# Performance work log

Measured on AMD Instinct MI355X. Metric: run time of the kernel, lower is better.

The kernel has to match this reference:

```python
import jax, jax.numpy as jnp
import numpy as np

N2 = 128      # time horizon (days)
M = 16384     # number of regions / batched chains
START = 6     # seeding window (days with externally seeded cases)


def setup_inputs() -> dict:
    key = jax.random.key(0)
    k0, k1, k2, k3, k4 = jax.random.split(key, 5)
    # reproduction numbers R_t in [0, 2)
    rt = jax.random.uniform(k0, (N2, M), dtype=jnp.float32) * 2.0
    deaths_gt = jax.random.uniform(k1, (N2, M), dtype=jnp.float32)
    # serial-interval distribution (positive, sums to 1 so the recurrence stays bounded)
    si_raw = jax.random.uniform(k2, (N2,), dtype=jnp.float32)
    SI = si_raw / jnp.sum(si_raw)
    f_raw = jax.random.uniform(k3, (N2, M), dtype=jnp.float32)
    f = f_raw / jnp.sum(f_raw, axis=0, keepdims=True) * 0.01
    # seeded cases for the first START days
    seed = jax.random.uniform(k4, (START, M), dtype=jnp.float32)
    return {"rt": rt, "deaths_gt": deaths_gt, "SI": SI, "f": f,
            "seed": seed, "start": START}


def _predict_cases(rt, SI, seed, start):
    # prediction[i, m] = rt[i, m] * sum_{j < i} prediction[j, m] * SI[i - j]
    # sequential triangular recurrence over time -> lax.scan with full carry.
    n2, m = rt.shape
    idx = jnp.arange(n2)
    pred0 = jnp.zeros((n2, m), rt.dtype).at[:start].set(seed)

    def step(pred, i):
        d = i - idx                                   # SI lag for each j
        w = jnp.where(d > 0, SI[jnp.clip(d, 0, n2 - 1)], 0.0)  # [N2], zero for j >= i
        conv = w @ pred                               # [M]
        row = jnp.where(i >= start, rt[i] * conv, pred[i])
        return pred.at[i].set(row), None

    pred, _ = jax.lax.scan(step, pred0, jnp.arange(n2))
    return pred


def _predict_deaths(pred, f, start):
    # E_deaths[i, m] = sum_{j <= i-2} pred[j, m] * f[i-j, m]
    # = causal per-region convolution with lags d = i-j >= 2 (so zero f[0], f[1]).
    n2, m = pred.shape
    f_eff = f.at[:2].set(0.0)
    conv = jax.vmap(lambda p, k: jnp.convolve(p, k)[:n2],
                    in_axes=1, out_axes=1)(pred, f_eff)   # [N2, M]
    i = jnp.arange(n2)[:, None]
    # rows before `start` are untouched by the loop (0), row 0 is set to 1e-9
    return jnp.where(i >= start, conv, jnp.where(i == 0, 1e-9, 0.0))


def reference(rt, deaths_gt, SI, f, seed, start):
    cases_pred = _predict_cases(rt, SI, seed, start)
    deaths_pred = _predict_deaths(cases_pred, f, start)
    return jnp.mean((deaths_pred - deaths_gt) ** 2)  # nn.MSELoss
```

## Files before the change

kernel.cpp:

```cpp
#include <hip/hip_runtime.h>

#define N2 128
#define MM 16384
#define START 6
#define CB 32
#define BT 256
#define PROWS 132
#define FROWS 152

__global__ __launch_bounds__(BT, 4) void npi_fused(
    const float* __restrict__ rt, const float* __restrict__ dgt,
    const float* __restrict__ si, const float* __restrict__ f,
    const float* __restrict__ seed, float* __restrict__ out)
{
    __shared__ float predT[PROWS * CB];
    __shared__ float funion[FROWS * CB];
    __shared__ float si_s[N2];
    __shared__ float lred[4];
    float* part = funion;
    float* fTd  = funion;

    const int t = threadIdx.x;
    const int c = t & (CB - 1);
    const int w = t >> 6;
    const int g = t >> 5;
    const int hw = g & 1;
    const int m = blockIdx.x * CB + c;

    float fregs[16];
#pragma unroll
    for (int q = 0; q < 16; ++q)
        fregs[q] = f[((g << 4) + q) * MM + m];

    if (t < N2) si_s[t] = si[t];
    if (g < START) predT[(g << 5) + c] = seed[g * MM + m];
    if (g < 4) predT[((128 + g) << 5) + c] = 0.f;

    float r16v[16];
#pragma unroll
    for (int k = 0; k < 16; ++k)
        r16v[k] = rt[k * MM + m];

    __syncthreads();

    float sr[16];
#pragma unroll
    for (int k = 1; k < 16; ++k) sr[k] = si_s[k];

    {
        float p_[16], v[16];
#pragma unroll
        for (int k = 0; k < 16; ++k) p_[k] = 0.f;
#pragma unroll
        for (int k = 0; k < 16; ++k) {
            float vk;
            if (k < START) vk = predT[(k << 5) + c];
            else vk = r16v[k] * (p_[k] + sr[1] * v[k - 1]);
            v[k] = vk;
#pragma unroll
            for (int k2 = k + 2; k2 < 16; ++k2)
                p_[k2] += sr[k2 - k] * vk;
        }
        if (w == 3 && hw == 0) {
#pragma unroll
            for (int k = START; k < 16; ++k) predT[(k << 5) + c] = v[k];
        }
    }
    __syncthreads();

    for (int b = 1; b < 8; ++b) {
        const int i0 = b << 4;
        const int nst = b << 1;
#pragma unroll
        for (int k = 0; k < 16; ++k)
            r16v[k] = rt[(i0 + k) * MM + m];

        const int jhi = nst * (g + 1);
        const int base = i0 - jhi + 1;
        float c16[16];
#pragma unroll
        for (int e = 0; e < 16; ++e) c16[e] = si_s[base + e];
        float acc[16];
#pragma unroll
        for (int k = 0; k < 16; ++k) acc[k] = 0.f;
#pragma unroll
        for (int u = 0; u < 14; ++u) {
            if (u < nst) {
                float p = predT[((jhi - 1 - u) << 5) + c];
#pragma unroll
                for (int k = 0; k < 16; ++k)
                    acc[k] += p * c16[(u + k) & 15];
                if (u + 1 < nst) c16[u & 15] = si_s[base + 16 + u];
            }
        }
#pragma unroll
        for (int k = 0; k < 16; ++k)
            acc[k] += __shfl_xor(acc[k], 32, 64);
        if (hw == 0) {
#pragma unroll
            for (int k = 0; k < 16; ++k)
                part[(((w << 4) + k) << 5) + c] = acc[k];
        }
        __syncthreads();

        float p_[16], v[16];
#pragma unroll
        for (int k = 0; k < 16; ++k)
            p_[k] = part[(k << 5) + c] + part[((16 + k) << 5) + c]
                  + part[((32 + k) << 5) + c] + part[((48 + k) << 5) + c];
#pragma unroll
        for (int k = 0; k < 16; ++k) {
            float vk = (k == 0) ? (r16v[0] * p_[0])
                                : (r16v[k] * (p_[k] + sr[1] * v[k - 1]));
            v[k] = vk;
#pragma unroll
            for (int k2 = k + 2; k2 < 16; ++k2)
                p_[k2] += sr[k2 - k] * vk;
        }
        {
            float a0, a1;
            if (w == 0)      { a0 = hw ? v[2]  : v[0];  a1 = hw ? v[3]  : v[1];  }
            else if (w == 1) { a0 = hw ? v[6]  : v[4];  a1 = hw ? v[7]  : v[5];  }
            else if (w == 2) { a0 = hw ? v[10] : v[8];  a1 = hw ? v[11] : v[9];  }
            else             { a0 = hw ? v[14] : v[12]; a1 = hw ? v[15] : v[13]; }
            const int r0 = i0 + (w << 2) + (hw << 1);
            predT[(r0 << 5) + c] = a0;
            predT[((r0 + 1) << 5) + c] = a1;
        }
        __syncthreads();
    }

#pragma unroll
    for (int q = 0; q < 16; ++q) {
        int d = (g << 4) + q;
        fTd[((16 + d) << 5) + c] = (d < 2) ? 0.f : fregs[q];
    }
    fTd[((g << 1) << 5) + c] = 0.f;
    fTd[(((g << 1) + 1) << 5) + c] = 0.f;
    fTd[((144 + g) << 5) + c] = 0.f;
    __syncthreads();

    float lsum = 0.f;
    if (hw == 0) {
        float dv = dgt[w * MM + m];
        float e0 = (w == 0) ? (1e-9f - dv) : dv;
        lsum += e0 * e0;
        if (w < 2) {
            float d2 = dgt[(4 + w) * MM + m];
            lsum += d2 * d2;
        }
    }

#pragma unroll
    for (int pass = 0; pass < 2; ++pass) {
        const int n = pass ? (7 - w) : w;
        const int i0 = START + (n << 4);
        const int jhi2 = i0 + 14;
        const int steps = jhi2 >> 1;
        const int jh = hw ? jhi2 : (jhi2 >> 1);
        const int fb = 17 + i0 - jh;

        float dg[16];
#pragma unroll
        for (int k = 0; k < 16; ++k)
            dg[k] = (i0 + k < N2) ? dgt[(i0 + k) * MM + m] : 0.f;

        float cf[16];
#pragma unroll
        for (int e = 0; e < 16; ++e) cf[e] = fTd[((fb + e) << 5) + c];
        float acc[16];
#pragma unroll
        for (int k = 0; k < 16; ++k) acc[k] = 0.f;

        for (int sb = 0; sb < steps; sb += 16) {
#pragma unroll
            for (int u = 0; u < 16; ++u) {
                int s = sb + u;
                if (s < steps) {
                    float p = predT[((jh - 1 - s) << 5) + c];
#pragma unroll
                    for (int k = 0; k < 16; ++k)
                        acc[k] += p * cf[(u + k) & 15];
                    cf[u] = fTd[((fb + 16 + s) << 5) + c];
                }
            }
        }
#pragma unroll
        for (int k = 0; k < 16; ++k)
            acc[k] += __shfl_xor(acc[k], 32, 64);
        if (hw == 0) {
#pragma unroll
            for (int k = 0; k < 16; ++k) {
                if (i0 + k < N2) {
                    float diff = acc[k] - dg[k];
                    lsum += diff * diff;
                }
            }
        }
    }

#pragma unroll
    for (int off = 32; off > 0; off >>= 1)
        lsum += __shfl_down(lsum, off, 64);
    if ((t & 63) == 0) lred[w] = lsum;
    __syncthreads();
    if (t == 0)
        atomicAdd(out, (lred[0] + lred[1] + lred[2] + lred[3]) *
                       (1.0f / ((float)N2 * (float)MM)));
}

extern "C" void kernel_launch(void* const* d_in, const int* in_sizes, int n_in,
                              void* d_out, int out_size, void* d_ws, size_t ws_size,
                              hipStream_t stream) {
    const float* rt   = (const float*)d_in[0];
    const float* dgt  = (const float*)d_in[1];
    const float* si   = (const float*)d_in[2];
    const float* f    = (const float*)d_in[3];
    const float* seed = (const float*)d_in[4];

    hipMemsetAsync(d_out, 0, sizeof(float), stream);
    npi_fused<<<dim3(MM / CB), dim3(BT), 0, stream>>>(
        rt, dgt, si, f, seed, (float*)d_out);
}
```

Before: 107.1 us.

## Halve columns per block and split convolution work four ways per column

Columns per block drop from 32 to 16, so each column is handled by 16 threads instead of 8. The j-range of the case and death convolutions is split four ways within a wavefront and reduced with two xor shuffles. The cross-wave partial sum moves into a separate shared-memory reduction pass with an extra barrier. Each thread now recomputes the 16-step recurrence but writes only one row, and loads of seed, death targets and f are spread across more threads. The intent is to double the number of blocks and cut the serial per-thread work for more parallelism and latency hiding, at the cost of more barriers, more shuffles and redundant recurrence work.

```diff
diff --git a/kernel.cpp b/kernel.cpp
--- a/kernel.cpp
+++ b/kernel.cpp
@@ -3,43 +3,42 @@
 #define N2 128
 #define MM 16384
 #define START 6
-#define CB 32
+#define CB 16
 #define BT 256
-#define PROWS 132
-#define FROWS 152
 
 __global__ __launch_bounds__(BT, 4) void npi_fused(
     const float* __restrict__ rt, const float* __restrict__ dgt,
     const float* __restrict__ si, const float* __restrict__ f,
     const float* __restrict__ seed, float* __restrict__ out)
 {
-    __shared__ float predT[PROWS * CB];
-    __shared__ float funion[FROWS * CB];
+    __shared__ float predT[132 * CB];
+    __shared__ float funion[152 * CB];
     __shared__ float si_s[N2];
     __shared__ float lred[4];
-    float* part = funion;
-    float* fTd  = funion;
 
     const int t = threadIdx.x;
-    const int c = t & (CB - 1);
+    const int c = t & 15;
+    const int s = (t >> 4) & 1;
+    const int h = (t >> 5) & 1;
     const int w = t >> 6;
-    const int g = t >> 5;
-    const int hw = g & 1;
+    const int q = (h << 1) | s;
+    const int g = (h << 3) | (w << 1) | s;
     const int m = blockIdx.x * CB + c;
 
-    float fregs[16];
-#pragma unroll
-    for (int q = 0; q < 16; ++q)
-        fregs[q] = f[((g << 4) + q) * MM + m];
+    float fregs[8];
+#pragma unroll
+    for (int r = 0; r < 8; ++r)
+        fregs[r] = f[((r << 4) + (t >> 4)) * MM + m];
 
     if (t < N2) si_s[t] = si[t];
-    if (g < START) predT[(g << 5) + c] = seed[g * MM + m];
-    if (g < 4) predT[((128 + g) << 5) + c] = 0.f;
-
-    float r16v[16];
-#pragma unroll
-    for (int k = 0; k < 16; ++k)
-        r16v[k] = rt[k * MM + m];
+    if (t < 64) predT[(128 + (t >> 4)) * CB + (t & 15)] = 0.f;
+
+    float sd[START];
+#pragma unroll
+    for (int k = 0; k < START; ++k) sd[k] = seed[k * MM + m];
+    float rtv[16];
+#pragma unroll
+    for (int k = 0; k < 16; ++k) rtv[k] = rt[k * MM + m];
 
     __syncthreads();
 
@@ -53,30 +52,25 @@
         for (int k = 0; k < 16; ++k) p_[k] = 0.f;
 #pragma unroll
         for (int k = 0; k < 16; ++k) {
-            float vk;
-            if (k < START) vk = predT[(k << 5) + c];
-            else vk = r16v[k] * (p_[k] + sr[1] * v[k - 1]);
+            float vk = (k < START) ? sd[k] : rtv[k] * (p_[k] + sr[1] * v[k - 1]);
             v[k] = vk;
 #pragma unroll
             for (int k2 = k + 2; k2 < 16; ++k2)
                 p_[k2] += sr[k2 - k] * vk;
         }
-        if (w == 3 && hw == 0) {
-#pragma unroll
-            for (int k = START; k < 16; ++k) predT[(k << 5) + c] = v[k];
-        }
+        const int row = (w << 2) + q;
+        predT[row * CB + c] = v[row];
     }
     __syncthreads();
 
     for (int b = 1; b < 8; ++b) {
         const int i0 = b << 4;
-        const int nst = b << 1;
 #pragma unroll
         for (int k = 0; k < 16; ++k)
-            r16v[k] = rt[(i0 + k) * MM + m];
-
-        const int jhi = nst * (g + 1);
-        const int base = i0 - jhi + 1;
+            rtv[k] = rt[(i0 + k) * MM + m];
+
+        const int jtop = b * (g + 1) - 1;
+        const int base = i0 - jtop;
         float c16[16];
 #pragma unroll
         for (int e = 0; e < 16; ++e) c16[e] = si_s[base + e];
@@ -84,69 +78,67 @@
 #pragma unroll
         for (int k = 0; k < 16; ++k) acc[k] = 0.f;
 #pragma unroll
-        for (int u = 0; u < 14; ++u) {
-            if (u < nst) {
-                float p = predT[((jhi - 1 - u) << 5) + c];
+        for (int u = 0; u < 7; ++u) {
+            if (u < b) {
+                float pv = predT[(jtop - u) * CB + c];
 #pragma unroll
                 for (int k = 0; k < 16; ++k)
-                    acc[k] += p * c16[(u + k) & 15];
-                if (u + 1 < nst) c16[u & 15] = si_s[base + 16 + u];
-            }
-        }
-#pragma unroll
-        for (int k = 0; k < 16; ++k)
+                    acc[k] += pv * c16[(u + k) & 15];
+                if (u + 1 < b) c16[u & 15] = si_s[base + 16 + u];
+            }
+        }
+#pragma unroll
+        for (int k = 0; k < 16; ++k) {
+            acc[k] += __shfl_xor(acc[k], 16, 64);
             acc[k] += __shfl_xor(acc[k], 32, 64);
-        if (hw == 0) {
+        }
+        if ((t & 48) == 0) {
 #pragma unroll
             for (int k = 0; k < 16; ++k)
-                part[(((w << 4) + k) << 5) + c] = acc[k];
+                funion[(w << 8) + (k << 4) + c] = acc[k];
         }
         __syncthreads();
 
-        float p_[16], v[16];
-#pragma unroll
-        for (int k = 0; k < 16; ++k)
-            p_[k] = part[(k << 5) + c] + part[((16 + k) << 5) + c]
-                  + part[((32 + k) << 5) + c] + part[((48 + k) << 5) + c];
-#pragma unroll
-        for (int k = 0; k < 16; ++k) {
-            float vk = (k == 0) ? (r16v[0] * p_[0])
-                                : (r16v[k] * (p_[k] + sr[1] * v[k - 1]));
-            v[k] = vk;
-#pragma unroll
-            for (int k2 = k + 2; k2 < 16; ++k2)
-                p_[k2] += sr[k2 - k] * vk;
-        }
+        funion[1024 + t] = funion[t] + funion[256 + t]
+                         + funion[512 + t] + funion[768 + t];
+        __syncthreads();
+
         {
-            float a0, a1;
-            if (w == 0)      { a0 = hw ? v[2]  : v[0];  a1 = hw ? v[3]  : v[1];  }
-            else if (w == 1) { a0 = hw ? v[6]  : v[4];  a1 = hw ? v[7]  : v[5];  }
-            else if (w == 2) { a0 = hw ? v[10] : v[8];  a1 = hw ? v[11] : v[9];  }
-            else             { a0 = hw ? v[14] : v[12]; a1 = hw ? v[15] : v[13]; }
-            const int r0 = i0 + (w << 2) + (hw << 1);
-            predT[(r0 << 5) + c] = a0;
-            predT[((r0 + 1) << 5) + c] = a1;
+            float p_[16], v[16];
+#pragma unroll
+            for (int k = 0; k < 16; ++k)
+                p_[k] = funion[1024 + (k << 4) + c];
+#pragma unroll
+            for (int k = 0; k < 16; ++k) {
+                float vk = (k == 0) ? (rtv[0] * p_[0])
+                                    : rtv[k] * (p_[k] + sr[1] * v[k - 1]);
+                v[k] = vk;
+#pragma unroll
+                for (int k2 = k + 2; k2 < 16; ++k2)
+                    p_[k2] += sr[k2 - k] * vk;
+            }
+            const int row = (w << 2) + q;
+            predT[(i0 + row) * CB + c] = v[row];
         }
         __syncthreads();
     }
 
-#pragma unroll
-    for (int q = 0; q < 16; ++q) {
-        int d = (g << 4) + q;
-        fTd[((16 + d) << 5) + c] = (d < 2) ? 0.f : fregs[q];
-    }
-    fTd[((g << 1) << 5) + c] = 0.f;
-    fTd[(((g << 1) + 1) << 5) + c] = 0.f;
-    fTd[((144 + g) << 5) + c] = 0.f;
+    funion[t] = 0.f;
+    if (t < 128) funion[2304 + t] = 0.f;
+#pragma unroll
+    for (int r = 0; r < 8; ++r) {
+        int d = (r << 4) + (t >> 4);
+        funion[(16 + d) * CB + c] = (d < 2) ? 0.f : fregs[r];
+    }
     __syncthreads();
 
     float lsum = 0.f;
-    if (hw == 0) {
-        float dv = dgt[w * MM + m];
-        float e0 = (w == 0) ? (1e-9f - dv) : dv;
+    if (w == 0) {
+        float dv = dgt[q * MM + m];
+        float e0 = (q == 0) ? (1e-9f - dv) : dv;
         lsum += e0 * e0;
-        if (w < 2) {
-            float d2 = dgt[(4 + w) * MM + m];
+        if (q < 2) {
+            float d2 = dgt[(4 + q) * MM + m];
             lsum += d2 * d2;
         }
     }
@@ -155,46 +147,50 @@
     for (int pass = 0; pass < 2; ++pass) {
         const int n = pass ? (7 - w) : w;
         const int i0 = START + (n << 4);
-        const int jhi2 = i0 + 14;
-        const int steps = jhi2 >> 1;
-        const int jh = hw ? jhi2 : (jhi2 >> 1);
-        const int fb = 17 + i0 - jh;
-
-        float dg[16];
-#pragma unroll
-        for (int k = 0; k < 16; ++k)
-            dg[k] = (i0 + k < N2) ? dgt[(i0 + k) * MM + m] : 0.f;
+        const int Q = 5 + (n << 2);
+        const int jtop = (q + 1) * Q - 1;
+        const int bidx = 16 + i0 - jtop;
+
+        float dgv[4];
+#pragma unroll
+        for (int r = 0; r < 4; ++r) {
+            int i = i0 + (q << 2) + r;
+            dgv[r] = (i < N2) ? dgt[i * MM + m] : 0.f;
+        }
 
         float cf[16];
 #pragma unroll
-        for (int e = 0; e < 16; ++e) cf[e] = fTd[((fb + e) << 5) + c];
+        for (int e = 0; e < 16; ++e) cf[e] = funion[(bidx + e) * CB + c];
         float acc[16];
 #pragma unroll
         for (int k = 0; k < 16; ++k) acc[k] = 0.f;
 
-        for (int sb = 0; sb < steps; sb += 16) {
+        for (int sb = 0; sb < Q; sb += 16) {
 #pragma unroll
             for (int u = 0; u < 16; ++u) {
-                int s = sb + u;
-                if (s < steps) {
-                    float p = predT[((jh - 1 - s) << 5) + c];
+                int sidx = sb + u;
+                if (sidx < Q) {
+                    float pv = predT[(jtop - sidx) * CB + c];
 #pragma unroll
                     for (int k = 0; k < 16; ++k)
-                        acc[k] += p * cf[(u + k) & 15];
-                    cf[u] = fTd[((fb + 16 + s) << 5) + c];
+                        acc[k] += pv * cf[(u + k) & 15];
+                    cf[u] = funion[(bidx + 16 + sidx) * CB + c];
                 }
             }
         }
 #pragma unroll
-        for (int k = 0; k < 16; ++k)
+        for (int k = 0; k < 16; ++k) {
+            acc[k] += __shfl_xor(acc[k], 16, 64);
             acc[k] += __shfl_xor(acc[k], 32, 64);
-        if (hw == 0) {
-#pragma unroll
-            for (int k = 0; k < 16; ++k) {
-                if (i0 + k < N2) {
-                    float diff = acc[k] - dg[k];
-                    lsum += diff * diff;
-                }
+        }
+#pragma unroll
+        for (int r = 0; r < 4; ++r) {
+            float av = (q == 0) ? acc[r] : (q == 1) ? acc[4 + r]
+                     : (q == 2) ? acc[8 + r] : acc[12 + r];
+            int i = i0 + (q << 2) + r;
+            if (i < N2) {
+                float diff = av - dgv[r];
+                lsum += diff * diff;
             }
         }
     }
```

Result: slower. 147.4 us (+37.7%).
